# Kernel optimization log

Measured on AMD Instinct MI355X. Metric: run time of the kernel, lower is better.

The kernel has to match this reference:

```python
import jax, jax.numpy as jnp
import numpy as np
import math

D_MODEL = 512
N_HEADS = 8
HEAD_DIM = D_MODEL // N_HEADS


def setup_inputs() -> dict:
    key = jax.random.key(0)
    k1, k2, k3 = jax.random.split(key, 3)
    B, T = 2, 4096
    x = jax.random.normal(k1, (B, T, D_MODEL), dtype=jnp.float32)
    # nn.Linear weights: stored as [out, in], applied as x @ W.T
    W_QKV = jax.random.normal(k2, (3 * D_MODEL, D_MODEL), dtype=jnp.float32) * (1.0 / math.sqrt(D_MODEL))
    W_O = jax.random.normal(k3, (D_MODEL, D_MODEL), dtype=jnp.float32) * (1.0 / math.sqrt(D_MODEL))
    return {"x": x, "W_QKV": W_QKV, "W_O": W_O}


def reference(x, W_QKV, W_O):
    B, T, C = x.shape
    qkv = (x @ W_QKV.T).reshape(B, T, 3, N_HEADS, HEAD_DIM)
    q, k, v = qkv[:, :, 0], qkv[:, :, 1], qkv[:, :, 2]  # [B,T,H,D]
    # scores: [B,H,T,T]
    scale = math.sqrt(HEAD_DIM)
    attn = jnp.einsum('bqhd,bkhd->bhqk', q, k) / scale
    causal_mask = jnp.triu(jnp.ones((T, T), dtype=bool), k=1)
    attn = jnp.where(causal_mask, -jnp.inf, attn)
    attn = jax.nn.softmax(attn, axis=-1)
    out = jnp.einsum('bhqk,bkhd->bqhd', attn, v).reshape(B, T, C)
    return out @ W_O.T
```

## Files before the change

kernel.cpp:

```cpp
#include <hip/hip_runtime.h>
#include <hip/hip_bf16.h>

typedef __bf16 bf16_t;
typedef __bf16 bf16x8 __attribute__((ext_vector_type(8)));
typedef __bf16 bf16x4 __attribute__((ext_vector_type(4)));
typedef float  floatx4 __attribute__((ext_vector_type(4)));

static __device__ __forceinline__ floatx4 mfma16(bf16x8 a, bf16x8 b, floatx4 c) {
  return __builtin_amdgcn_mfma_f32_16x16x32_bf16(a, b, c, 0, 0, 0);
}

typedef __attribute__((address_space(3))) void lds_vp;
typedef __attribute__((address_space(1))) void glb_vp;
#define GLDS16(g, l) \
  __builtin_amdgcn_global_load_lds((glb_vp*)(g), (lds_vp*)(l), 16, 0, 0)

__global__ void cvt_all_kernel(const float* __restrict__ x,
                               const float* __restrict__ wqkv,
                               const float* __restrict__ wo,
                               bf16_t* __restrict__ xb,
                               bf16_t* __restrict__ wqkvb,
                               bf16_t* __restrict__ wob) {
  int i = blockIdx.x * blockDim.x + threadIdx.x;
  const float4* src; bf16x4* dst; int off;
  if (i < 1048576)      { src = (const float4*)x;    dst = (bf16x4*)xb;    off = i; }
  else if (i < 1245184) { src = (const float4*)wqkv; dst = (bf16x4*)wqkvb; off = i - 1048576; }
  else                  { src = (const float4*)wo;   dst = (bf16x4*)wob;   off = i - 1245184; }
  float4 v = src[off];
  bf16x4 o;
  o[0] = (bf16_t)v.x; o[1] = (bf16_t)v.y; o[2] = (bf16_t)v.z; o[3] = (bf16_t)v.w;
  dst[off] = o;
}

__global__ __launch_bounds__(256) void gemm_qkv(
    const bf16_t* __restrict__ A, const bf16_t* __restrict__ B,
    bf16_t* __restrict__ Qo, bf16_t* __restrict__ Ko, bf16_t* __restrict__ Vto)
{
  __shared__ __align__(16) bf16_t As[2][128 * 64];
  __shared__ __align__(16) bf16_t Bs[2][128 * 64];
  const int tid  = threadIdx.x;
  const int lane = tid & 63;
  const int w    = tid >> 6;
  const int quad = lane >> 4;
  const int l15  = lane & 15;
  const int l7   = lane & 7;
  const int wm   = w & 1;
  const int wn   = w >> 1;
  const int K    = 512;

  floatx4 acc[4][4];
  #pragma unroll
  for (int i = 0; i < 4; ++i)
    #pragma unroll
    for (int j = 0; j < 4; ++j)
      acc[i][j] = (floatx4){0.f, 0.f, 0.f, 0.f};

  const bf16_t* Ab = A + (size_t)blockIdx.x * 128 * K;
  const bf16_t* Bb = B + (size_t)blockIdx.y * 128 * K;

  auto stage = [&](int buf, int k0) {
    #pragma unroll
    for (int i = 0; i < 4; ++i) {
      int c = tid + 256 * i;
      int row = c >> 3, colc = c & 7;
      int gofs = ((colc ^ (row & 7)) << 3);
      GLDS16(&Ab[(size_t)row * K + k0 + gofs], &As[buf][c * 8]);
      GLDS16(&Bb[(size_t)row * K + k0 + gofs], &Bs[buf][c * 8]);
    }
  };

  stage(0, 0);
  for (int it = 0; it < 8; ++it) {
    const int cur = it & 1;
    __syncthreads();
    if (it + 1 < 8) stage(cur ^ 1, (it + 1) << 6);
    #pragma unroll
    for (int ks = 0; ks < 2; ++ks) {
      bf16x8 af[4], bfr[4];
      #pragma unroll
      for (int t = 0; t < 4; ++t) {
        af[t]  = *(const bf16x8*)&As[cur][(wm * 64 + t * 16 + l15) * 64 +
                                         (((ks * 4 + quad) ^ l7) << 3)];
        bfr[t] = *(const bf16x8*)&Bs[cur][(wn * 64 + t * 16 + l15) * 64 +
                                         (((ks * 4 + quad) ^ l7) << 3)];
      }
      #pragma unroll
      for (int mt = 0; mt < 4; ++mt)
        #pragma unroll
        for (int nt = 0; nt < 4; ++nt)
          acc[mt][nt] = mfma16(af[mt], bfr[nt], acc[mt][nt]);
    }
  }

  if (blockIdx.y < 8) {
    #pragma unroll
    for (int mt = 0; mt < 4; ++mt) {
      #pragma unroll
      for (int nt = 0; nt < 4; ++nt) {
        #pragma unroll
        for (int r = 0; r < 4; ++r) {
          int m = blockIdx.x * 128 + wm * 64 + mt * 16 + quad * 4 + r;
          int n = blockIdx.y * 128 + wn * 64 + nt * 16 + l15;
          float v = acc[mt][nt][r];
          int b = m >> 12, t = m & 4095;
          int h = (n >> 6) & 7, d = n & 63;
          size_t bh = (size_t)(b * 8 + h);
          if (n < 512)
            Qo[bh * 262144 + (size_t)t * 64 + d] = (bf16_t)(v * 0.18033688f);
          else
            Ko[bh * 262144 + (size_t)t * 64 + d] = (bf16_t)v;
        }
      }
    }
  } else {
    __syncthreads();
    bf16_t* L = &As[0][0];
    #pragma unroll
    for (int mt = 0; mt < 4; ++mt)
      #pragma unroll
      for (int nt = 0; nt < 4; ++nt) {
        int n_l = wn * 64 + nt * 16 + l15;
        int mc  = wm * 8 + mt * 2 + (quad >> 1);
        bf16x4 v4;
        #pragma unroll
        for (int r = 0; r < 4; ++r) v4[r] = (bf16_t)acc[mt][nt][r];
        *(bf16x4*)&L[n_l * 128 + ((mc ^ (n_l & 15)) << 3) + (quad & 1) * 4] = v4;
      }
    __syncthreads();
    const int t0 = (blockIdx.x & 31) * 128;
    const int b  = blockIdx.x >> 5;
    #pragma unroll
    for (int i = 0; i < 8; ++i) {
      int c = tid + 256 * i;
      int n_l = c >> 4, tc = c & 15;
      int h = ((blockIdx.y - 8) << 1) | (n_l >> 6);
      int d = n_l & 63;
      size_t bh = (size_t)(b * 8 + h);
      int base0 = (tc >> 2) * 32 + (tc & 3) * 4;
      bf16x4 lo = *(const bf16x4*)&L[n_l * 128 +
                     (((base0 >> 3) ^ (n_l & 15)) << 3) + (base0 & 7)];
      bf16x4 hi = *(const bf16x4*)&L[n_l * 128 +
                     ((((base0 + 16) >> 3) ^ (n_l & 15)) << 3) + (base0 & 7)];
      bf16x8 o;
      #pragma unroll
      for (int e = 0; e < 4; ++e) { o[e] = lo[e]; o[e + 4] = hi[e]; }
      *(bf16x8*)&Vto[bh * 262144 + (size_t)d * 4096 + t0 + tc * 8] = o;
    }
  }
}

__global__ __launch_bounds__(256) void gemm_out(
    const bf16_t* __restrict__ A, const bf16_t* __restrict__ B,
    float* __restrict__ Cf)
{
  __shared__ __align__(16) bf16_t As[2][64 * 64];
  __shared__ __align__(16) bf16_t Bs[2][128 * 64];
  const int tid  = threadIdx.x;
  const int lane = tid & 63;
  const int w    = tid >> 6;
  const int quad = lane >> 4;
  const int l15  = lane & 15;
  const int l7   = lane & 7;

  floatx4 acc[4][2];
  #pragma unroll
  for (int i = 0; i < 4; ++i)
    #pragma unroll
    for (int j = 0; j < 2; ++j)
      acc[i][j] = (floatx4){0.f, 0.f, 0.f, 0.f};

  const bf16_t* Ab = A + (size_t)blockIdx.x * 64 * 512;
  const bf16_t* Bb = B + (size_t)blockIdx.y * 128 * 512;

  auto stage = [&](int buf, int k0) {
    #pragma unroll
    for (int i = 0; i < 2; ++i) {
      int c = tid + 256 * i;
      int row = c >> 3, colc = c & 7;
      GLDS16(&Ab[(size_t)row * 512 + k0 + ((colc ^ (row & 7)) << 3)],
             &As[buf][c * 8]);
    }
    #pragma unroll
    for (int i = 0; i < 4; ++i) {
      int c = tid + 256 * i;
      int row = c >> 3, colc = c & 7;
      GLDS16(&Bb[(size_t)row * 512 + k0 + ((colc ^ (row & 7)) << 3)],
             &Bs[buf][c * 8]);
    }
  };

  stage(0, 0);
  for (int it = 0; it < 8; ++it) {
    const int cur = it & 1;
    __syncthreads();
    if (it + 1 < 8) stage(cur ^ 1, (it + 1) << 6);
    #pragma unroll
    for (int ks = 0; ks < 2; ++ks) {
      bf16x8 af[4], bfr[2];
      #pragma unroll
      for (int t = 0; t < 4; ++t)
        af[t]  = *(const bf16x8*)&As[cur][(t * 16 + l15) * 64 +
                                         (((ks * 4 + quad) ^ l7) << 3)];
      #pragma unroll
      for (int t = 0; t < 2; ++t)
        bfr[t] = *(const bf16x8*)&Bs[cur][(w * 32 + t * 16 + l15) * 64 +
                                         (((ks * 4 + quad) ^ l7) << 3)];
      #pragma unroll
      for (int mt = 0; mt < 4; ++mt)
        #pragma unroll
        for (int nt = 0; nt < 2; ++nt)
          acc[mt][nt] = mfma16(af[mt], bfr[nt], acc[mt][nt]);
    }
  }

  #pragma unroll
  for (int mt = 0; mt < 4; ++mt)
    #pragma unroll
    for (int nt = 0; nt < 2; ++nt)
      #pragma unroll
      for (int r = 0; r < 4; ++r) {
        int m = blockIdx.x * 64 + mt * 16 + quad * 4 + r;
        int n = blockIdx.y * 128 + w * 32 + nt * 16 + l15;
        Cf[(size_t)m * 512 + n] = acc[mt][nt][r];
      }
}

__global__ __launch_bounds__(256, 4) void attn_kernel(
    const bf16_t* __restrict__ Qg, const bf16_t* __restrict__ Kgl,
    const bf16_t* __restrict__ Vtg, bf16_t* __restrict__ Og)
{
  __shared__ __align__(16) bf16_t smem[32768];
  bf16_t* KsB  = smem;
  bf16_t* VtsB = smem + 16384;

  const int tid  = threadIdx.x;
  const int lane = tid & 63;
  const int w    = tid >> 6;
  const int qh   = w >> 1;
  const int kh   = w & 1;
  const int quad = lane >> 4;
  const int l15  = lane & 15;

  const int id = blockIdx.x;
  const int qt = 31 - (id >> 4);
  const int bh = 2 * (id & 7) + ((id >> 3) & 1);
  const int qt2  = qt * 2 + qh;
  const size_t bh_off = (size_t)bh * 262144;
  const int b = bh >> 3, h = bh & 7;

  const int qbase = qt * 128 + qh * 64;
  bf16x8 aq0[4], aq1[4];
  #pragma unroll
  for (int qb = 0; qb < 4; ++qb) {
    const bf16_t* Qp = Qg + bh_off + (size_t)(qbase + qb * 16 + l15) * 64;
    aq0[qb] = *(const bf16x8*)&Qp[quad * 8];
    aq1[qb] = *(const bf16x8*)&Qp[32 + quad * 8];
  }
  bf16x8 ones;
  #pragma unroll
  for (int i = 0; i < 8; ++i) ones[i] = (bf16_t)1.0f;

  floatx4 acc_o[4][4], acc_l[4];
  #pragma unroll
  for (int qb = 0; qb < 4; ++qb) {
    #pragma unroll
    for (int dt = 0; dt < 4; ++dt) acc_o[qb][dt] = (floatx4){0.f, 0.f, 0.f, 0.f};
    acc_l[qb] = (floatx4){0.f, 0.f, 0.f, 0.f};
  }

  auto stage = [&](int buf, int kt) {
    const bf16_t* Kp = Kgl + bh_off + (size_t)kt * 8192;
    const bf16_t* Vp = Vtg + bh_off + (size_t)kt * 128;
    #pragma unroll
    for (int i = 0; i < 4; ++i) {
      int c = tid + 256 * i;
      int row = c >> 3, colc = c & 7;
      GLDS16(&Kp[row * 64 + ((colc ^ (row & 7)) << 3)], &KsB[buf * 8192 + c * 8]);
    }
    #pragma unroll
    for (int i = 0; i < 4; ++i) {
      int c = tid + 256 * i;
      int row = c >> 4, colc = c & 15;
      GLDS16(&Vp[(size_t)row * 4096 + ((colc ^ (row & 15)) << 3)],
             &VtsB[buf * 8192 + c * 8]);
    }
  };

  stage(0, 0);
  const int nkt = qt + 1;
  const floatx4 z4 = (floatx4){0.f, 0.f, 0.f, 0.f};
  for (int kt = 0; kt < nkt; ++kt) {
    const int cur = kt & 1;
    __syncthreads();
    if (kt + 1 < nkt) stage(cur ^ 1, kt + 1);

    if (2 * kt + kh <= qt2) {
      const bf16_t* Kc = &KsB[cur * 8192 + kh * 64 * 64];
      const bf16_t* Vc = &VtsB[cur * 8192];
      floatx4 s[4][4];
      #pragma unroll
      for (int nt = 0; nt < 4; ++nt) {
        bf16x8 bk0 = *(const bf16x8*)&Kc[(nt * 16 + l15) * 64 +
                                         ((quad ^ (l15 & 7)) << 3)];
        s[0][nt] = mfma16(bk0, aq0[0], z4);
        s[1][nt] = mfma16(bk0, aq0[1], z4);
        s[2][nt] = mfma16(bk0, aq0[2], z4);
        s[3][nt] = mfma16(bk0, aq0[3], z4);
      }
      #pragma unroll
      for (int nt = 0; nt < 4; ++nt) {
        bf16x8 bk1 = *(const bf16x8*)&Kc[(nt * 16 + l15) * 64 +
                                         (((4 + quad) ^ (l15 & 7)) << 3)];
        #pragma unroll
        for (int qb = 0; qb < 4; ++qb)
          s[qb][nt] = mfma16(bk1, aq1[qb], s[qb][nt]);
      }

      if (2 * kt + kh == qt2) {
        #pragma unroll
        for (int qb = 0; qb < 4; ++qb)
          #pragma unroll
          for (int nt = 0; nt < 4; ++nt)
            #pragma unroll
            for (int r = 0; r < 4; ++r)
              if (nt * 16 + quad * 4 + r > qb * 16 + l15)
                s[qb][nt][r] = -3.0e38f;
      }
      #pragma unroll
      for (int qb = 0; qb < 4; ++qb)
        #pragma unroll
        for (int nt = 0; nt < 4; ++nt)
          #pragma unroll
          for (int r = 0; r < 4; ++r)
            s[qb][nt][r] = __builtin_amdgcn_exp2f(s[qb][nt][r]);

      #pragma unroll
      for (int kc = 0; kc < 2; ++kc) {
        bf16x8 pb[4];
        #pragma unroll
        for (int qb = 0; qb < 4; ++qb)
          #pragma unroll
          for (int r = 0; r < 4; ++r) {
            pb[qb][r]     = (bf16_t)s[qb][kc * 2][r];
            pb[qb][r + 4] = (bf16_t)s[qb][kc * 2 + 1][r];
          }
        #pragma unroll
        for (int qb = 0; qb < 4; ++qb)
          acc_l[qb] = mfma16(ones, pb[qb], acc_l[qb]);
        #pragma unroll
        for (int dt = 0; dt < 4; ++dt) {
          bf16x8 av = *(const bf16x8*)&Vc[(dt * 16 + l15) * 128 +
                         ((((kh * 2 + kc) * 4 + quad) ^ l15) << 3)];
          #pragma unroll
          for (int qb = 0; qb < 4; ++qb)
            acc_o[qb][dt] = mfma16(av, pb[qb], acc_o[qb][dt]);
        }
      }
    }
  }

  __syncthreads();
  float*  PART = (float*)smem;
  bf16_t* OUT  = smem + 16640;
  const int p = qh;
  float* P = PART + p * 4160;

  if (kh == 1) {
    #pragma unroll
    for (int qb = 0; qb < 4; ++qb) {
      #pragma unroll
      for (int dt = 0; dt < 4; ++dt) {
        int chunk = (dt * 4 + quad) ^ l15;
        *(floatx4*)&P[(qb * 16 + l15) * 64 + chunk * 4] = acc_o[qb][dt];
      }
      if (quad == 0) P[4096 + qb * 16 + l15] = acc_l[qb][0];
    }
  }
  __syncthreads();
  if (kh == 0) {
    bf16_t* Ot = OUT + p * 4096;
    #pragma unroll
    for (int qb = 0; qb < 4; ++qb) {
      const int t_own = qb * 16 + l15;
      float rl = 1.0f / (acc_l[qb][0] + P[4096 + t_own]);
      #pragma unroll
      for (int dt = 0; dt < 4; ++dt) {
        int chunk = (dt * 4 + quad) ^ l15;
        floatx4 pp = *(const floatx4*)&P[t_own * 64 + chunk * 4];
        bf16x4 o4;
        #pragma unroll
        for (int r = 0; r < 4; ++r)
          o4[r] = (bf16_t)((acc_o[qb][dt][r] + pp[r]) * rl);
        *(bf16x4*)&Ot[t_own * 64 +
                      (((dt * 2 + (quad >> 1)) ^ (t_own & 7)) << 3) +
                      (quad & 1) * 4] = o4;
      }
    }
  }
  __syncthreads();
  {
    bf16_t* Ot = OUT + p * 4096;
    const int gtid = (kh << 6) | lane;
    #pragma unroll
    for (int i = 0; i < 4; ++i) {
      int cc = gtid + 128 * i;
      int t = cc >> 3, c = cc & 7;
      bf16x8 o8 = *(const bf16x8*)&Ot[t * 64 + ((c ^ (t & 7)) << 3)];
      int trow = qbase + t;
      *(bf16x8*)&Og[((size_t)b * 4096 + trow) * 512 + h * 64 + c * 8] = o8;
    }
  }
}

extern "C" void kernel_launch(void* const* d_in, const int* in_sizes, int n_in,
                              void* d_out, int out_size, void* d_ws, size_t ws_size,
                              hipStream_t stream) {
  const float* x    = (const float*)d_in[0];
  const float* wqkv = (const float*)d_in[1];
  const float* wo   = (const float*)d_in[2];
  float* out = (float*)d_out;

  char* ws = (char*)d_ws;
  bf16_t* xb    = (bf16_t*)(ws);
  bf16_t* wqkvb = (bf16_t*)(ws + 8388608);
  bf16_t* wob   = (bf16_t*)(ws + 9961472);
  bf16_t* Qb    = (bf16_t*)(ws + 10485760);
  bf16_t* Kb    = (bf16_t*)(ws + 18874368);
  bf16_t* Vtb   = (bf16_t*)(ws + 27262976);
  bf16_t* Ob    = xb;

  cvt_all_kernel<<<5120, 256, 0, stream>>>(x, wqkv, wo, xb, wqkvb, wob);

  gemm_qkv<<<dim3(64, 12), 256, 0, stream>>>(xb, wqkvb, Qb, Kb, Vtb);
  attn_kernel<<<dim3(512), 256, 0, stream>>>(Qb, Kb, Vtb, Ob);
  gemm_out<<<dim3(128, 4), 256, 0, stream>>>(Ob, wob, out);
}
```

Baseline: 165.6 us.

## Pair heavy and light causal query tiles per block with 4-way key split

Each block now handles two 64-row query tiles (a long one from the end and a short one from the start), so every block runs the same fixed 33 key iterations, which balances the causal triangle across blocks. Within a block the four waves split each 128-key tile four ways (32 keys each) instead of 2 query halves × 2 key halves, and the partial outputs are reduced through LDS in a multi-step epilogue. Launch bounds drop to 2 blocks per CU and LDS grows. The cost is more epilogue reductions and synchronisations, and less occupancy.

```diff
diff --git a/kernel.cpp b/kernel.cpp
--- a/kernel.cpp
+++ b/kernel.cpp
@@ -225,48 +225,51 @@
       }
 }
 
-__global__ __launch_bounds__(256, 4) void attn_kernel(
+__global__ __launch_bounds__(256, 2) void attn_kernel(
     const bf16_t* __restrict__ Qg, const bf16_t* __restrict__ Kgl,
     const bf16_t* __restrict__ Vtg, bf16_t* __restrict__ Og)
 {
-  __shared__ __align__(16) bf16_t smem[32768];
-  bf16_t* KsB  = smem;
-  bf16_t* VtsB = smem + 16384;
+  __shared__ __align__(16) bf16_t smem[36928];
 
   const int tid  = threadIdx.x;
   const int lane = tid & 63;
-  const int w    = tid >> 6;
-  const int qh   = w >> 1;
-  const int kh   = w & 1;
+  const int kq   = tid >> 6;
   const int quad = lane >> 4;
   const int l15  = lane & 15;
+  const int l7   = lane & 7;
 
   const int id = blockIdx.x;
-  const int qt = 31 - (id >> 4);
   const int bh = 2 * (id & 7) + ((id >> 3) & 1);
-  const int qt2  = qt * 2 + qh;
+  const int y  = id >> 4;
+  const int qA = 63 - y, qB = y;
+  const int NA = (65 - y) >> 1;
   const size_t bh_off = (size_t)bh * 262144;
   const int b = bh >> 3, h = bh & 7;
 
-  const int qbase = qt * 128 + qh * 64;
   bf16x8 aq0[4], aq1[4];
-  #pragma unroll
-  for (int qb = 0; qb < 4; ++qb) {
-    const bf16_t* Qp = Qg + bh_off + (size_t)(qbase + qb * 16 + l15) * 64;
-    aq0[qb] = *(const bf16x8*)&Qp[quad * 8];
-    aq1[qb] = *(const bf16x8*)&Qp[32 + quad * 8];
-  }
+  auto loadQ = [&](int q64) {
+    #pragma unroll
+    for (int qb = 0; qb < 4; ++qb) {
+      const bf16_t* Qp = Qg + bh_off + (size_t)(q64 * 64 + qb * 16 + l15) * 64;
+      aq0[qb] = *(const bf16x8*)&Qp[quad * 8];
+      aq1[qb] = *(const bf16x8*)&Qp[32 + quad * 8];
+    }
+  };
+
   bf16x8 ones;
   #pragma unroll
   for (int i = 0; i < 8; ++i) ones[i] = (bf16_t)1.0f;
 
   floatx4 acc_o[4][4], acc_l[4];
-  #pragma unroll
-  for (int qb = 0; qb < 4; ++qb) {
-    #pragma unroll
-    for (int dt = 0; dt < 4; ++dt) acc_o[qb][dt] = (floatx4){0.f, 0.f, 0.f, 0.f};
-    acc_l[qb] = (floatx4){0.f, 0.f, 0.f, 0.f};
-  }
+  auto zacc = [&]() {
+    #pragma unroll
+    for (int qb = 0; qb < 4; ++qb) {
+      #pragma unroll
+      for (int dt = 0; dt < 4; ++dt) acc_o[qb][dt] = (floatx4){0.f, 0.f, 0.f, 0.f};
+      acc_l[qb] = (floatx4){0.f, 0.f, 0.f, 0.f};
+    }
+  };
+  zacc();
 
   auto stage = [&](int buf, int kt) {
     const bf16_t* Kp = Kgl + bh_off + (size_t)kt * 8192;
@@ -275,141 +278,164 @@
     for (int i = 0; i < 4; ++i) {
       int c = tid + 256 * i;
       int row = c >> 3, colc = c & 7;
-      GLDS16(&Kp[row * 64 + ((colc ^ (row & 7)) << 3)], &KsB[buf * 8192 + c * 8]);
+      GLDS16(&Kp[row * 64 + ((colc ^ (row & 7)) << 3)], &smem[buf * 8192 + c * 8]);
     }
     #pragma unroll
     for (int i = 0; i < 4; ++i) {
       int c = tid + 256 * i;
       int row = c >> 4, colc = c & 15;
       GLDS16(&Vp[(size_t)row * 4096 + ((colc ^ (row & 15)) << 3)],
-             &VtsB[buf * 8192 + c * 8]);
-    }
-  };
-
-  stage(0, 0);
-  const int nkt = qt + 1;
-  const floatx4 z4 = (floatx4){0.f, 0.f, 0.f, 0.f};
-  for (int kt = 0; kt < nkt; ++kt) {
-    const int cur = kt & 1;
-    __syncthreads();
-    if (kt + 1 < nkt) stage(cur ^ 1, kt + 1);
-
-    if (2 * kt + kh <= qt2) {
-      const bf16_t* Kc = &KsB[cur * 8192 + kh * 64 * 64];
-      const bf16_t* Vc = &VtsB[cur * 8192];
-      floatx4 s[4][4];
-      #pragma unroll
-      for (int nt = 0; nt < 4; ++nt) {
-        bf16x8 bk0 = *(const bf16x8*)&Kc[(nt * 16 + l15) * 64 +
-                                         ((quad ^ (l15 & 7)) << 3)];
-        s[0][nt] = mfma16(bk0, aq0[0], z4);
-        s[1][nt] = mfma16(bk0, aq0[1], z4);
-        s[2][nt] = mfma16(bk0, aq0[2], z4);
-        s[3][nt] = mfma16(bk0, aq0[3], z4);
-      }
-      #pragma unroll
-      for (int nt = 0; nt < 4; ++nt) {
-        bf16x8 bk1 = *(const bf16x8*)&Kc[(nt * 16 + l15) * 64 +
-                                         (((4 + quad) ^ (l15 & 7)) << 3)];
-        #pragma unroll
-        for (int qb = 0; qb < 4; ++qb)
-          s[qb][nt] = mfma16(bk1, aq1[qb], s[qb][nt]);
-      }
-
-      if (2 * kt + kh == qt2) {
-        #pragma unroll
-        for (int qb = 0; qb < 4; ++qb)
-          #pragma unroll
-          for (int nt = 0; nt < 4; ++nt)
+             &smem[16384 + buf * 8192 + c * 8]);
+    }
+  };
+
+  auto epi = [&](int q64) {
+    float*  P    = (float*)&smem[32768];
+    float*  PL   = (float*)&smem[36864];
+    bf16_t* OUTb = &smem[32768];
+    #pragma unroll
+    for (int hf = 0; hf < 2; ++hf) {
+      __syncthreads();
+      if (kq == 3) {
+        #pragma unroll
+        for (int q2 = 0; q2 < 2; ++q2) {
+          int qb = hf * 2 + q2, t32 = q2 * 16 + l15;
+          #pragma unroll
+          for (int dt = 0; dt < 4; ++dt)
+            *(floatx4*)&P[t32 * 64 + (((dt * 4 + quad) ^ l15) << 2)] = acc_o[qb][dt];
+          if (quad == 0) PL[t32] = acc_l[qb][0];
+        }
+      }
+      __syncthreads();
+      #pragma unroll
+      for (int src = 2; src >= 1; --src) {
+        if (kq == src) {
+          #pragma unroll
+          for (int q2 = 0; q2 < 2; ++q2) {
+            int qb = hf * 2 + q2, t32 = q2 * 16 + l15;
+            floatx4 tmp[4];
+            #pragma unroll
+            for (int dt = 0; dt < 4; ++dt)
+              tmp[dt] = *(const floatx4*)&P[t32 * 64 + (((dt * 4 + quad) ^ l15) << 2)];
+            float tl = PL[t32];
+            #pragma unroll
+            for (int dt = 0; dt < 4; ++dt)
+              *(floatx4*)&P[t32 * 64 + (((dt * 4 + quad) ^ l15) << 2)] =
+                  tmp[dt] + acc_o[qb][dt];
+            if (quad == 0) PL[t32] = tl + acc_l[qb][0];
+          }
+        }
+        __syncthreads();
+      }
+      if (kq == 0) {
+        #pragma unroll
+        for (int q2 = 0; q2 < 2; ++q2) {
+          int qb = hf * 2 + q2, t32 = q2 * 16 + l15;
+          floatx4 tmp[4];
+          #pragma unroll
+          for (int dt = 0; dt < 4; ++dt)
+            tmp[dt] = *(const floatx4*)&P[t32 * 64 + (((dt * 4 + quad) ^ l15) << 2)];
+          float rl = 1.0f / (acc_l[qb][0] + PL[t32]);
+          #pragma unroll
+          for (int dt = 0; dt < 4; ++dt) {
+            bf16x4 o4;
             #pragma unroll
             for (int r = 0; r < 4; ++r)
-              if (nt * 16 + quad * 4 + r > qb * 16 + l15)
+              o4[r] = (bf16_t)((acc_o[qb][dt][r] + tmp[dt][r]) * rl);
+            *(bf16x4*)&OUTb[t32 * 64 +
+                            (((dt * 2 + (quad >> 1)) ^ (t32 & 7)) << 3) +
+                            (quad & 1) * 4] = o4;
+          }
+        }
+      }
+      __syncthreads();
+      {
+        int t = tid >> 3, c = tid & 7;
+        bf16x8 o8 = *(const bf16x8*)&OUTb[t * 64 + ((c ^ (t & 7)) << 3)];
+        int row = q64 * 64 + hf * 32 + t;
+        *(bf16x8*)&Og[((size_t)b * 4096 + row) * 512 + h * 64 + c * 8] = o8;
+      }
+    }
+  };
+
+  const floatx4 z4 = (floatx4){0.f, 0.f, 0.f, 0.f};
+  loadQ(qA);
+  stage(0, 0);
+  for (int g = 0; g < 33; ++g) {
+    const int cur = g & 1;
+    __syncthreads();
+    if (g == NA) {
+      epi(qA);
+      zacc();
+      loadQ(qB);
+    }
+    if (g + 1 < 33) {
+      int s = g + 1;
+      stage(cur ^ 1, (s < NA) ? s : s - NA);
+    }
+    const int kt  = (g < NA) ? g : g - NA;
+    const int q64 = (g < NA) ? qA : qB;
+    const int rel = (4 * kt + kq) * 32 - q64 * 64;
+    if (rel <= 32) {
+      const bf16_t* Kc = &smem[cur * 8192];
+      const bf16_t* Vc = &smem[16384 + cur * 8192];
+      floatx4 s[4][2];
+      #pragma unroll
+      for (int nt = 0; nt < 2; ++nt) {
+        bf16x8 bk = *(const bf16x8*)&Kc[(kq * 32 + nt * 16 + l15) * 64 +
+                                        ((quad ^ l7) << 3)];
+        s[0][nt] = mfma16(bk, aq0[0], z4);
+        s[1][nt] = mfma16(bk, aq0[1], z4);
+        s[2][nt] = mfma16(bk, aq0[2], z4);
+        s[3][nt] = mfma16(bk, aq0[3], z4);
+      }
+      #pragma unroll
+      for (int nt = 0; nt < 2; ++nt) {
+        bf16x8 bk = *(const bf16x8*)&Kc[(kq * 32 + nt * 16 + l15) * 64 +
+                                        (((4 + quad) ^ l7) << 3)];
+        #pragma unroll
+        for (int qb = 0; qb < 4; ++qb)
+          s[qb][nt] = mfma16(bk, aq1[qb], s[qb][nt]);
+      }
+      if (rel >= 0) {
+        #pragma unroll
+        for (int qb = 0; qb < 4; ++qb)
+          #pragma unroll
+          for (int nt = 0; nt < 2; ++nt)
+            #pragma unroll
+            for (int r = 0; r < 4; ++r)
+              if (rel + nt * 16 + quad * 4 + r > qb * 16 + l15)
                 s[qb][nt][r] = -3.0e38f;
       }
       #pragma unroll
       for (int qb = 0; qb < 4; ++qb)
         #pragma unroll
-        for (int nt = 0; nt < 4; ++nt)
+        for (int nt = 0; nt < 2; ++nt)
           #pragma unroll
           for (int r = 0; r < 4; ++r)
             s[qb][nt][r] = __builtin_amdgcn_exp2f(s[qb][nt][r]);
-
-      #pragma unroll
-      for (int kc = 0; kc < 2; ++kc) {
-        bf16x8 pb[4];
+      bf16x8 pb[4];
+      #pragma unroll
+      for (int qb = 0; qb < 4; ++qb)
+        #pragma unroll
+        for (int r = 0; r < 4; ++r) {
+          pb[qb][r]     = (bf16_t)s[qb][0][r];
+          pb[qb][r + 4] = (bf16_t)s[qb][1][r];
+        }
+      #pragma unroll
+      for (int qb = 0; qb < 4; ++qb)
+        acc_l[qb] = mfma16(ones, pb[qb], acc_l[qb]);
+      #pragma unroll
+      for (int dt = 0; dt < 4; ++dt) {
+        bf16x8 av = *(const bf16x8*)&Vc[(dt * 16 + l15) * 128 +
+                                        (((kq * 4 + quad) ^ l15) << 3)];
         #pragma unroll
         for (int qb = 0; qb < 4; ++qb)
-          #pragma unroll
-          for (int r = 0; r < 4; ++r) {
-            pb[qb][r]     = (bf16_t)s[qb][kc * 2][r];
-            pb[qb][r + 4] = (bf16_t)s[qb][kc * 2 + 1][r];
-          }
-        #pragma unroll
-        for (int qb = 0; qb < 4; ++qb)
-          acc_l[qb] = mfma16(ones, pb[qb], acc_l[qb]);
-        #pragma unroll
-        for (int dt = 0; dt < 4; ++dt) {
-          bf16x8 av = *(const bf16x8*)&Vc[(dt * 16 + l15) * 128 +
-                         ((((kh * 2 + kc) * 4 + quad) ^ l15) << 3)];
-          #pragma unroll
-          for (int qb = 0; qb < 4; ++qb)
-            acc_o[qb][dt] = mfma16(av, pb[qb], acc_o[qb][dt]);
-        }
+          acc_o[qb][dt] = mfma16(av, pb[qb], acc_o[qb][dt]);
       }
     }
   }
-
-  __syncthreads();
-  float*  PART = (float*)smem;
-  bf16_t* OUT  = smem + 16640;
-  const int p = qh;
-  float* P = PART + p * 4160;
-
-  if (kh == 1) {
-    #pragma unroll
-    for (int qb = 0; qb < 4; ++qb) {
-      #pragma unroll
-      for (int dt = 0; dt < 4; ++dt) {
-        int chunk = (dt * 4 + quad) ^ l15;
-        *(floatx4*)&P[(qb * 16 + l15) * 64 + chunk * 4] = acc_o[qb][dt];
-      }
-      if (quad == 0) P[4096 + qb * 16 + l15] = acc_l[qb][0];
-    }
-  }
-  __syncthreads();
-  if (kh == 0) {
-    bf16_t* Ot = OUT + p * 4096;
-    #pragma unroll
-    for (int qb = 0; qb < 4; ++qb) {
-      const int t_own = qb * 16 + l15;
-      float rl = 1.0f / (acc_l[qb][0] + P[4096 + t_own]);
-      #pragma unroll
-      for (int dt = 0; dt < 4; ++dt) {
-        int chunk = (dt * 4 + quad) ^ l15;
-        floatx4 pp = *(const floatx4*)&P[t_own * 64 + chunk * 4];
-        bf16x4 o4;
-        #pragma unroll
-        for (int r = 0; r < 4; ++r)
-          o4[r] = (bf16_t)((acc_o[qb][dt][r] + pp[r]) * rl);
-        *(bf16x4*)&Ot[t_own * 64 +
-                      (((dt * 2 + (quad >> 1)) ^ (t_own & 7)) << 3) +
-                      (quad & 1) * 4] = o4;
-      }
-    }
-  }
-  __syncthreads();
-  {
-    bf16_t* Ot = OUT + p * 4096;
-    const int gtid = (kh << 6) | lane;
-    #pragma unroll
-    for (int i = 0; i < 4; ++i) {
-      int cc = gtid + 128 * i;
-      int t = cc >> 3, c = cc & 7;
-      bf16x8 o8 = *(const bf16x8*)&Ot[t * 64 + ((c ^ (t & 7)) << 3)];
-      int trow = qbase + t;
-      *(bf16x8*)&Og[((size_t)b * 4096 + trow) * 512 + h * 64 + c * 8] = o8;
-    }
-  }
+  epi(qB);
 }
 
 extern "C" void kernel_launch(void* const* d_in, const int* in_sizes, int n_in,
```

New measurement: 153.0 us. 7.6% less time.
